# Performance work log

Hardware: AMD Instinct MI355X
Metric: run time of the kernel (lower is better)

Reference implementation:

```python
import jax, jax.numpy as jnp
import numpy as np

N_PATCHES = 16
PATCH_H = 128
PATCH_W = 128
RECEPTIVE_FIELD = 0


def setup_inputs() -> dict:
    key = jax.random.key(0)
    k1, k2, k3, k4 = jax.random.split(key, 4)
    B, HL, WL, HH, WH, C = 16, 128, 128, 1024, 1024, 3
    x_low = jax.random.normal(k1, (B, HL, WL, C), dtype=jnp.float32)
    x_high = jax.random.normal(k2, (B, HH, WH, C), dtype=jnp.float32)
    # attention is a probability map over the low-res spatial grid
    att = jax.random.uniform(k3, (B, HL, WL), dtype=jnp.float32, minval=1e-3, maxval=1.0)
    att = att / jnp.sum(att, axis=(1, 2), keepdims=True)
    # pre-drawn Gumbel noise for sampling-without-replacement (Gumbel top-k)
    u = jax.random.uniform(k4, (B, HL * WL), dtype=jnp.float32, minval=1e-6, maxval=1.0 - 1e-6)
    gumbel = -jnp.log(-jnp.log(u))
    return {"x_low": x_low, "x_high": x_high, "attention": att, "gumbel_noise": gumbel}


def reference(x_low, x_high, attention, gumbel_noise):
    B, HL, WL = attention.shape
    HH, WH, C = x_high.shape[1], x_high.shape[2], x_high.shape[3]

    # --- sample(n_patches, attention, sample_space, replace=False, use_logits=False) ---
    flat_att = attention.reshape(B, HL * WL)
    logits = jnp.log(flat_att)  # use_logits=False -> log(probs)
    # Gumbel top-k == sampling n_patches indices without replacement
    _, idx = jax.lax.top_k(logits + gumbel_noise, N_PATCHES)  # [B, n_patches] int32
    sampled_attention = jnp.take_along_axis(flat_att, idx, axis=1)  # [B, n_patches]
    si = idx // WL  # row index in sample_space
    sj = idx % WL   # col index in sample_space

    # --- map sample_space coords -> low-res coords -> high-res coords ---
    # sample_space spans (shape(x_low)[1:-1] - receptive_field) pixels of x_low;
    # with receptive_field=0 this is identity, offsets = receptive_field/2 = 0.
    HL_eff = HL  # = x_low spatial - receptive_field
    WL_eff = WL
    off = RECEPTIVE_FIELD / 2.0
    p_h = si.astype(jnp.float32) * (HL_eff / HL) + off  # low-res coords
    p_w = sj.astype(jnp.float32) * (WL_eff / WL) + off
    scale_h = HH / x_low.shape[1]
    scale_w = WH / x_low.shape[2]
    top = jnp.clip(jnp.round(p_h * scale_h).astype(jnp.int32), 0, HH - PATCH_H)
    left = jnp.clip(jnp.round(p_w * scale_w).astype(jnp.int32), 0, WH - PATCH_W)

    # --- gather patches from x_high (irregular coordinate-based crop) ---
    def extract_one(img, t, l):
        return jax.lax.dynamic_slice(img, (t, l, 0), (PATCH_H, PATCH_W, C))

    def extract_batch_elem(img, ts, ls):
        return jax.vmap(lambda t, l: extract_one(img, t, l))(ts, ls)

    patches = jax.vmap(extract_batch_elem)(x_high, top, left)  # [B, n, ph, pw, C]
    return patches, sampled_attention
```

## Files before the change

kernel.cpp:

```cpp
#include <hip/hip_runtime.h>

#define BATCH 16
#define HL 128
#define WL 128
#define HH 1024
#define WH 1024
#define CH 3
#define NP 16
#define PH 128
#define PW 128

#define TOTAL4 (BATCH * NP * PH * PW * CH / 4)
#define F4_PER_THREAD 8

__global__ __launch_bounds__(256) void topk_kernel(
    const float* __restrict__ att,
    const float* __restrict__ gum,
    float* __restrict__ out_att,
    int* __restrict__ tops,
    int* __restrict__ lefts)
{
    const int b   = blockIdx.x;
    const int tid = threadIdx.x;
    const float* a = att + (size_t)b * (HL * WL);
    const float* g = gum + (size_t)b * (HL * WL);

    float sc[64];
#pragma unroll
    for (int t = 0; t < 64; ++t) {
        const int e = tid + t * 256;
        sc[t] = logf(a[e]) + g[e];
    }

    __shared__ float s_val[4];
    __shared__ int   s_idx[4];
    __shared__ int   s_win;

    unsigned long long taken = 0ULL;
    const int lane = tid & 63;
    const int wave = tid >> 6;

    for (int r = 0; r < NP; ++r) {
        float best = -3.0e38f;
        int   bidx = 0x7fffffff;
#pragma unroll
        for (int t = 0; t < 64; ++t) {
            if (!((taken >> t) & 1ULL)) {
                const float v = sc[t];
                const int   e = tid + t * 256;
                if (v > best || (v == best && e < bidx)) { best = v; bidx = e; }
            }
        }
#pragma unroll
        for (int off = 32; off; off >>= 1) {
            const float ov = __shfl_down(best, off);
            const int   oi = __shfl_down(bidx, off);
            if (ov > best || (ov == best && oi < bidx)) { best = ov; bidx = oi; }
        }
        if (lane == 0) { s_val[wave] = best; s_idx[wave] = bidx; }
        __syncthreads();
        if (tid == 0) {
            float bv = s_val[0];
            int   bi = s_idx[0];
#pragma unroll
            for (int w = 1; w < 4; ++w) {
                if (s_val[w] > bv || (s_val[w] == bv && s_idx[w] < bi)) {
                    bv = s_val[w]; bi = s_idx[w];
                }
            }
            s_win = bi;
            const int si = bi / WL;
            const int sj = bi % WL;
            int t_ = si * 8; if (t_ > HH - PH) t_ = HH - PH;
            int l_ = sj * 8; if (l_ > WH - PW) l_ = WH - PW;
            tops[b * NP + r]  = t_;
            lefts[b * NP + r] = l_;
            out_att[b * NP + r] = a[bi];
        }
        __syncthreads();
        const int win = s_win;
        if ((win & 255) == tid) taken |= 1ULL << (win >> 8);
    }
}

__global__ __launch_bounds__(256) void gather_kernel(
    const float* __restrict__ xh,
    const int* __restrict__ tops,
    const int* __restrict__ lefts,
    float* __restrict__ out)
{
    const int base = blockIdx.x * (256 * F4_PER_THREAD) + threadIdx.x;
#pragma unroll
    for (int s = 0; s < F4_PER_THREAD; ++s) {
        const int j4 = base + s * 256;
        const int lane = j4 % 96;
        const int row  = j4 / 96;
        const int b    = row >> 11;
        const int rem  = row & 2047;
        const int n    = rem >> 7;
        const int ph   = rem & 127;
        const int tl   = (b << 4) + n;
        const int top  = tops[tl];
        const int left = lefts[tl];
        const size_t src4 = (size_t)(b * HH + top + ph) * (WH * CH / 4)
                          + ((left * CH) >> 2) + lane;
        ((float4*)out)[j4] = ((const float4*)xh)[src4];
    }
}

extern "C" void kernel_launch(void* const* d_in, const int* in_sizes, int n_in,
                              void* d_out, int out_size, void* d_ws, size_t ws_size,
                              hipStream_t stream) {
    const float* xh  = (const float*)d_in[1];
    const float* att = (const float*)d_in[2];
    const float* gum = (const float*)d_in[3];

    float* out_patches = (float*)d_out;
    float* out_att     = (float*)d_out + (size_t)BATCH * NP * PH * PW * CH;

    int* tops  = (int*)d_ws;
    int* lefts = (int*)d_ws + BATCH * NP;

    topk_kernel<<<BATCH, 256, 0, stream>>>(att, gum, out_att, tops, lefts);

    gather_kernel<<<TOTAL4 / (256 * F4_PER_THREAD), 256, 0, stream>>>(
        xh, tops, lefts, out_patches);
}
```

Baseline: 342.2 us.

## Widen top-k block to 1024 threads with incremental rescan; nontemporal gather copies

The top-k kernel now runs 1024 threads per batch element with 16 scores each. Only the thread that owned the winner rescans its candidates, and a shuffle reduction across 16 waves replaces the serial thread-0 loop. The gather kernel switches to nontemporal vector loads and stores and doubles the float4s handled per thread. These changes target the serial latency of the 16 selection rounds and cache pollution from streaming copies, at the cost of fewer gather blocks and larger top-k blocks.

```diff
diff --git a/kernel.cpp b/kernel.cpp
--- a/kernel.cpp
+++ b/kernel.cpp
@@ -10,10 +10,13 @@
 #define PH 128
 #define PW 128
 
+#define NEL (HL * WL)
 #define TOTAL4 (BATCH * NP * PH * PW * CH / 4)
-#define F4_PER_THREAD 8
+#define F4_PER_THREAD 16
 
-__global__ __launch_bounds__(256) void topk_kernel(
+typedef float f32x4 __attribute__((ext_vector_type(4)));
+
+__global__ __launch_bounds__(1024) void topk_kernel(
     const float* __restrict__ att,
     const float* __restrict__ gum,
     float* __restrict__ out_att,
@@ -22,64 +25,72 @@
 {
     const int b   = blockIdx.x;
     const int tid = threadIdx.x;
-    const float* a = att + (size_t)b * (HL * WL);
-    const float* g = gum + (size_t)b * (HL * WL);
+    const float* a = att + (size_t)b * NEL;
+    const float* g = gum + (size_t)b * NEL;
 
-    float sc[64];
+    float sc[16];
 #pragma unroll
-    for (int t = 0; t < 64; ++t) {
-        const int e = tid + t * 256;
+    for (int t = 0; t < 16; ++t) {
+        const int e = tid + t * 1024;
         sc[t] = logf(a[e]) + g[e];
     }
 
-    __shared__ float s_val[4];
-    __shared__ int   s_idx[4];
+    unsigned taken = 0;
+    float best; int bidx;
+    auto rescan = [&]() {
+        best = -3.0e38f; bidx = 0x7fffffff;
+#pragma unroll
+        for (int t = 0; t < 16; ++t) {
+            if (!((taken >> t) & 1u)) {
+                const float v = sc[t];
+                const int   e = tid + t * 1024;
+                if (v > best || (v == best && e < bidx)) { best = v; bidx = e; }
+            }
+        }
+    };
+    rescan();
+
+    __shared__ float s_val[16];
+    __shared__ int   s_idx[16];
     __shared__ int   s_win;
-
-    unsigned long long taken = 0ULL;
     const int lane = tid & 63;
     const int wave = tid >> 6;
 
     for (int r = 0; r < NP; ++r) {
-        float best = -3.0e38f;
-        int   bidx = 0x7fffffff;
-#pragma unroll
-        for (int t = 0; t < 64; ++t) {
-            if (!((taken >> t) & 1ULL)) {
-                const float v = sc[t];
-                const int   e = tid + t * 256;
-                if (v > best || (v == best && e < bidx)) { best = v; bidx = e; }
-            }
-        }
+        float wb = best; int wi = bidx;
 #pragma unroll
         for (int off = 32; off; off >>= 1) {
-            const float ov = __shfl_down(best, off);
-            const int   oi = __shfl_down(bidx, off);
-            if (ov > best || (ov == best && oi < bidx)) { best = ov; bidx = oi; }
+            const float ov = __shfl_down(wb, off);
+            const int   oi = __shfl_down(wi, off);
+            if (ov > wb || (ov == wb && oi < wi)) { wb = ov; wi = oi; }
         }
-        if (lane == 0) { s_val[wave] = best; s_idx[wave] = bidx; }
+        if (lane == 0) { s_val[wave] = wb; s_idx[wave] = wi; }
         __syncthreads();
-        if (tid == 0) {
-            float bv = s_val[0];
-            int   bi = s_idx[0];
+        if (wave == 0 && lane < 16) {
+            float v = s_val[lane]; int i = s_idx[lane];
 #pragma unroll
-            for (int w = 1; w < 4; ++w) {
-                if (s_val[w] > bv || (s_val[w] == bv && s_idx[w] < bi)) {
-                    bv = s_val[w]; bi = s_idx[w];
-                }
+            for (int off = 8; off; off >>= 1) {
+                const float ov = __shfl_xor(v, off, 16);
+                const int   oi = __shfl_xor(i, off, 16);
+                if (ov > v || (ov == v && oi < i)) { v = ov; i = oi; }
             }
-            s_win = bi;
-            const int si = bi / WL;
-            const int sj = bi % WL;
-            int t_ = si * 8; if (t_ > HH - PH) t_ = HH - PH;
-            int l_ = sj * 8; if (l_ > WH - PW) l_ = WH - PW;
-            tops[b * NP + r]  = t_;
-            lefts[b * NP + r] = l_;
-            out_att[b * NP + r] = a[bi];
+            if (lane == 0) {
+                s_win = i;
+                const int si = i >> 7;
+                const int sj = i & 127;
+                int t_ = si * 8; if (t_ > HH - PH) t_ = HH - PH;
+                int l_ = sj * 8; if (l_ > WH - PW) l_ = WH - PW;
+                tops[b * NP + r]  = t_;
+                lefts[b * NP + r] = l_;
+                out_att[b * NP + r] = a[i];
+            }
         }
         __syncthreads();
         const int win = s_win;
-        if ((win & 255) == tid) taken |= 1ULL << (win >> 8);
+        if ((win & 1023) == tid) {
+            taken |= 1u << (win >> 10);
+            rescan();
+        }
     }
 }
 
@@ -104,7 +115,8 @@
         const int left = lefts[tl];
         const size_t src4 = (size_t)(b * HH + top + ph) * (WH * CH / 4)
                           + ((left * CH) >> 2) + lane;
-        ((float4*)out)[j4] = ((const float4*)xh)[src4];
+        const f32x4 v = __builtin_nontemporal_load(((const f32x4*)xh) + src4);
+        __builtin_nontemporal_store(v, ((f32x4*)out) + j4);
     }
 }
 
@@ -121,7 +133,7 @@
     int* tops  = (int*)d_ws;
     int* lefts = (int*)d_ws + BATCH * NP;
 
-    topk_kernel<<<BATCH, 256, 0, stream>>>(att, gum, out_att, tops, lefts);
+    topk_kernel<<<BATCH, 1024, 0, stream>>>(att, gum, out_att, tops, lefts);
 
     gather_kernel<<<TOTAL4 / (256 * F4_PER_THREAD), 256, 0, stream>>>(
         xh, tops, lefts, out_patches);
```

New measurement: 292.9 us. -14.4%, faster.
